# Optimization experiments

Measured on AMD Instinct MI355X. Metric: run time of the kernel, lower is better.

Reference implementation:

```python
import jax, jax.numpy as jnp
import numpy as np

N_NODES = 100000
N_EDGES = 1600000
H_FEATS = 128
OUT_CLASSES = 6


def setup_inputs() -> dict:
    key = jax.random.key(0)
    ks = jax.random.split(key, 9)
    h = jax.random.normal(ks[0], (N_NODES, H_FEATS), dtype=jnp.float32)
    src = jax.random.randint(ks[1], (N_EDGES,), 0, N_NODES)
    dst = jax.random.randint(ks[2], (N_EDGES,), 0, N_NODES)
    # torch nn.Linear convention: y = x @ W.T + b, W shape [out, in]
    W1 = jax.random.normal(ks[3], (64, 2 * H_FEATS), dtype=jnp.float32) * 0.05
    b1 = jax.random.normal(ks[4], (64,), dtype=jnp.float32) * 0.05
    W2 = jax.random.normal(ks[5], (32, 64), dtype=jnp.float32) * 0.05
    b2 = jax.random.normal(ks[6], (32,), dtype=jnp.float32) * 0.05
    W3 = jax.random.normal(ks[7], (OUT_CLASSES, 32), dtype=jnp.float32) * 0.05
    b3 = jax.random.normal(ks[8], (OUT_CLASSES,), dtype=jnp.float32) * 0.05
    return {"h": h, "src": src, "dst": dst, "W1": W1, "b1": b1,
            "W2": W2, "b2": b2, "W3": W3, "b3": b3}


def reference(h, src, dst, W1, b1, W2, b2, W3, b3):
    # Per-edge gather of src/dst node features, concat -> [E, 2*H]
    x = jnp.concatenate([h[src], h[dst]], axis=1)
    x = jax.nn.relu(x @ W1.T + b1)   # [E, 64]
    x = jax.nn.relu(x @ W2.T + b2)   # [E, 32]
    return x @ W3.T + b3             # [E, output_class]
```

## Files before the change

### kernel.cpp

```cpp
#include <hip/hip_runtime.h>
#include <hip/hip_bf16.h>
#include <stdint.h>


#define H 128

typedef short bf16x8 __attribute__((ext_vector_type(8)));
typedef float f32x4  __attribute__((ext_vector_type(4)));

__device__ __forceinline__ uint16_t f2bf(float f) {
    uint32_t u = __float_as_uint(f);
    return (uint16_t)((u + 0x7fffu + ((u >> 16) & 1u)) >> 16);
}
__device__ __forceinline__ float bf_lo(uint32_t u) { return __uint_as_float(u << 16); }
__device__ __forceinline__ float bf_hi(uint32_t u) { return __uint_as_float(u & 0xffff0000u); }
__device__ __forceinline__ uint32_t pk_bf16(float lo, float hi) {
    __hip_bfloat162 v = __float22bfloat162_rn(float2{lo, hi});
    return *reinterpret_cast<uint32_t*>(&v);
}

__global__ void prep_weights(const float* __restrict__ W1,
                             const float* __restrict__ W2,
                             const float* __restrict__ W3,
                             uint16_t* __restrict__ Bfrag,
                             uint16_t* __restrict__ EFrag)
{
    int t = blockIdx.x * blockDim.x + threadIdx.x;
    int stride = gridDim.x * blockDim.x;
    for (int i = t; i < 4 * 8 * 64 * 8; i += stride) {
        int j    = i & 7;
        int lane = (i >> 3) & 63;
        int nt   = (i >> 9) & 7;
        int kt   = (i >> 12);
        int k = kt * 32 + (lane >> 4) * 8 + j;
        int n = nt * 16 + (lane & 15);
        float v = (n < 64) ? W1[n * 256 + k] : W1[(n - 64) * 256 + 128 + k];
        Bfrag[i] = f2bf(v);
    }
    for (int i = t; i < 5 * 64 * 8; i += stride) {
        int j    = i & 7;
        int lane = (i >> 3) & 63;
        int f    = i >> 9;
        uint16_t v;
        if (f < 4) {
            int kt = f >> 1, nt = f & 1;
            int k = kt * 32 + (lane >> 4) * 8 + j;
            int n = nt * 16 + (lane & 15);
            v = f2bf(W2[n * 64 + k]);
        } else {
            int k = (lane >> 4) * 8 + j;
            int n = lane & 15;
            v = (n < 6) ? f2bf(W3[n * 32 + k]) : (uint16_t)0;
        }
        EFrag[i] = v;
    }
}

__global__ void __launch_bounds__(256) node_gemm(
    const float* __restrict__ h,
    const uint16_t* __restrict__ Bfrag,
    const float* __restrict__ b1,
    uint16_t* __restrict__ pre, int N)
{
    const int wave = threadIdx.x >> 6;
    const int lane = threadIdx.x & 63;
    const int n0 = (blockIdx.x * 4 + wave) * 16;
    if (n0 >= N) return;

    const int m    = lane & 15;
    const int quad = lane >> 4;

    int arow = n0 + m; if (arow >= N) arow = N - 1;
    const float* hrow = h + (size_t)arow * H + quad * 8;

    bf16x8 afr[4];
#pragma unroll
    for (int kt = 0; kt < 4; kt++) {
        float4 lo = *(const float4*)(hrow + kt * 32);
        float4 hi = *(const float4*)(hrow + kt * 32 + 4);
        bf16x8 a;
        a[0] = (short)f2bf(lo.x); a[1] = (short)f2bf(lo.y);
        a[2] = (short)f2bf(lo.z); a[3] = (short)f2bf(lo.w);
        a[4] = (short)f2bf(hi.x); a[5] = (short)f2bf(hi.y);
        a[6] = (short)f2bf(hi.z); a[7] = (short)f2bf(hi.w);
        afr[kt] = a;
    }

#pragma unroll
    for (int nt = 0; nt < 8; nt++) {
        f32x4 acc = {0.f, 0.f, 0.f, 0.f};
#pragma unroll
        for (int kt = 0; kt < 4; kt++) {
            bf16x8 bfr = *(const bf16x8*)(Bfrag + ((size_t)(kt * 8 + nt) * 64 + lane) * 8);
            acc = __builtin_amdgcn_mfma_f32_16x16x32_bf16(afr[kt], bfr, acc, 0, 0, 0);
        }
        const int ncol = nt * 16 + m;
        const float bv = (ncol < 64) ? b1[ncol] : 0.f;
#pragma unroll
        for (int r = 0; r < 4; r++) {
            const int node = n0 + quad * 4 + r;
            if (node < N)
                pre[(size_t)node * H + ncol] = f2bf(acc[r] + bv);
        }
    }
}

__global__ void __launch_bounds__(256, 2) edge_mlp(
    const uint16_t* __restrict__ pre,
    const int* __restrict__ src, const int* __restrict__ dst,
    const uint16_t* __restrict__ EFrag,
    const float* __restrict__ b2, const float* __restrict__ b3,
    float* __restrict__ out, long E)
{
    __shared__ uint16_t zbuf[4][64 * 40];

    const int wave = threadIdx.x >> 6;
    const int lane = threadIdx.x & 63;
    const int m15  = lane & 15;
    const int quad = lane >> 4;
    uint16_t* zw = &zbuf[wave][0];

    bf16x8 bL2[4], bL3;
#pragma unroll
    for (int f = 0; f < 4; f++) bL2[f] = *(const bf16x8*)(EFrag + (f * 64 + lane) * 8);
    bL3 = *(const bf16x8*)(EFrag + (4 * 64 + lane) * 8);
    const float vb2a = b2[m15];
    const float vb2b = b2[16 + m15];
    const float vb3  = (m15 < 6) ? b3[m15] : 0.f;

    const long e0 = (long)(blockIdx.x * 4 + wave) * 64;
    if (e0 >= E) return;

#pragma unroll
    for (int st = 0; st < 4; st++) {
        long e = e0 + st * 16 + m15;
        if (e >= E) e = E - 1;
        const int se = src[e], de = dst[e];
        const uint16_t* pa = pre + (size_t)se * H;
        const uint16_t* pb = pre + (size_t)de * H + 64;

        bf16x8 afr[2];
#pragma unroll
        for (int kt = 0; kt < 2; kt++) {
            uint4 ua = *(const uint4*)(pa + kt * 32 + quad * 8);
            uint4 ub = *(const uint4*)(pb + kt * 32 + quad * 8);
            float y0 = fmaxf(bf_lo(ua.x) + bf_lo(ub.x), 0.f);
            float y1 = fmaxf(bf_hi(ua.x) + bf_hi(ub.x), 0.f);
            float y2 = fmaxf(bf_lo(ua.y) + bf_lo(ub.y), 0.f);
            float y3 = fmaxf(bf_hi(ua.y) + bf_hi(ub.y), 0.f);
            float y4 = fmaxf(bf_lo(ua.z) + bf_lo(ub.z), 0.f);
            float y5 = fmaxf(bf_hi(ua.z) + bf_hi(ub.z), 0.f);
            float y6 = fmaxf(bf_lo(ua.w) + bf_lo(ub.w), 0.f);
            float y7 = fmaxf(bf_hi(ua.w) + bf_hi(ub.w), 0.f);
            union { bf16x8 v; uint32_t u[4]; } A;
            A.u[0] = pk_bf16(y0, y1);
            A.u[1] = pk_bf16(y2, y3);
            A.u[2] = pk_bf16(y4, y5);
            A.u[3] = pk_bf16(y6, y7);
            afr[kt] = A.v;
        }

#pragma unroll
        for (int nt = 0; nt < 2; nt++) {
            f32x4 acc = {0.f, 0.f, 0.f, 0.f};
            acc = __builtin_amdgcn_mfma_f32_16x16x32_bf16(afr[0], bL2[0 * 2 + nt], acc, 0, 0, 0);
            acc = __builtin_amdgcn_mfma_f32_16x16x32_bf16(afr[1], bL2[1 * 2 + nt], acc, 0, 0, 0);
            const float vb2 = nt ? vb2b : vb2a;
#pragma unroll
            for (int r = 0; r < 4; r++) {
                float z = fmaxf(acc[r] + vb2, 0.f);
                int el = st * 16 + quad * 4 + r;
                zw[el * 40 + nt * 16 + m15] = f2bf(z);
            }
        }
    }

#pragma unroll
    for (int st = 0; st < 4; st++) {
        bf16x8 a3 = *(const bf16x8*)(zw + (st * 16 + m15) * 40 + quad * 8);
        f32x4 o = {0.f, 0.f, 0.f, 0.f};
        o = __builtin_amdgcn_mfma_f32_16x16x32_bf16(a3, bL3, o, 0, 0, 0);
        if (m15 < 6) {
#pragma unroll
            for (int r = 0; r < 4; r++) {
                long e = e0 + st * 16 + quad * 4 + r;
                if (e < E) out[e * 6 + m15] = o[r] + vb3;
            }
        }
    }
}

extern "C" void kernel_launch(void* const* d_in, const int* in_sizes, int n_in,
                              void* d_out, int out_size, void* d_ws, size_t ws_size,
                              hipStream_t stream) {
    const float* h   = (const float*)d_in[0];
    const int*   src = (const int*)d_in[1];
    const int*   dst = (const int*)d_in[2];
    const float* W1  = (const float*)d_in[3];
    const float* b1  = (const float*)d_in[4];
    const float* W2  = (const float*)d_in[5];
    const float* b2  = (const float*)d_in[6];
    const float* W3  = (const float*)d_in[7];
    const float* b3  = (const float*)d_in[8];

    const int  N = in_sizes[0] / H;
    const long E = in_sizes[1];

    char* ws = (char*)d_ws;
    uint16_t* Bfrag = (uint16_t*)ws;
    uint16_t* EFrag = (uint16_t*)(ws + 64 * 1024);
    uint16_t* pre   = (uint16_t*)(ws + 128 * 1024);

    prep_weights<<<64, 256, 0, stream>>>(W1, W2, W3, Bfrag, EFrag);
    node_gemm<<<(N + 63) / 64, 256, 0, stream>>>(h, Bfrag, b1, pre, N);
    const int eblocks = (int)((E + 255) / 256);
    edge_mlp<<<eblocks, 256, 0, stream>>>(pre, src, dst, EFrag, b2, b3,
                                          (float*)d_out, E);
}
```

Before: 188.3 us.

## Drop weight-prep kernel and software-pipeline edge gathers over 128 edges per wave

Result: slower. 230.3 us (+22.3%).

```diff
diff --git a/kernel.cpp b/kernel.cpp
--- a/kernel.cpp
+++ b/kernel.cpp
@@ -18,47 +18,18 @@
     __hip_bfloat162 v = __float22bfloat162_rn(float2{lo, hi});
     return *reinterpret_cast<uint32_t*>(&v);
 }
-
-__global__ void prep_weights(const float* __restrict__ W1,
-                             const float* __restrict__ W2,
-                             const float* __restrict__ W3,
-                             uint16_t* __restrict__ Bfrag,
-                             uint16_t* __restrict__ EFrag)
-{
-    int t = blockIdx.x * blockDim.x + threadIdx.x;
-    int stride = gridDim.x * blockDim.x;
-    for (int i = t; i < 4 * 8 * 64 * 8; i += stride) {
-        int j    = i & 7;
-        int lane = (i >> 3) & 63;
-        int nt   = (i >> 9) & 7;
-        int kt   = (i >> 12);
-        int k = kt * 32 + (lane >> 4) * 8 + j;
-        int n = nt * 16 + (lane & 15);
-        float v = (n < 64) ? W1[n * 256 + k] : W1[(n - 64) * 256 + 128 + k];
-        Bfrag[i] = f2bf(v);
-    }
-    for (int i = t; i < 5 * 64 * 8; i += stride) {
-        int j    = i & 7;
-        int lane = (i >> 3) & 63;
-        int f    = i >> 9;
-        uint16_t v;
-        if (f < 4) {
-            int kt = f >> 1, nt = f & 1;
-            int k = kt * 32 + (lane >> 4) * 8 + j;
-            int n = nt * 16 + (lane & 15);
-            v = f2bf(W2[n * 64 + k]);
-        } else {
-            int k = (lane >> 4) * 8 + j;
-            int n = lane & 15;
-            v = (n < 6) ? f2bf(W3[n * 32 + k]) : (uint16_t)0;
-        }
-        EFrag[i] = v;
-    }
+__device__ __forceinline__ bf16x8 pack_frag(float4 lo, float4 hi) {
+    union { bf16x8 v; uint32_t u[4]; } A;
+    A.u[0] = pk_bf16(lo.x, lo.y);
+    A.u[1] = pk_bf16(lo.z, lo.w);
+    A.u[2] = pk_bf16(hi.x, hi.y);
+    A.u[3] = pk_bf16(hi.z, hi.w);
+    return A.v;
 }
 
 __global__ void __launch_bounds__(256) node_gemm(
     const float* __restrict__ h,
-    const uint16_t* __restrict__ Bfrag,
+    const float* __restrict__ W1,
     const float* __restrict__ b1,
     uint16_t* __restrict__ pre, int N)
 {
@@ -78,29 +49,33 @@
     for (int kt = 0; kt < 4; kt++) {
         float4 lo = *(const float4*)(hrow + kt * 32);
         float4 hi = *(const float4*)(hrow + kt * 32 + 4);
-        bf16x8 a;
-        a[0] = (short)f2bf(lo.x); a[1] = (short)f2bf(lo.y);
-        a[2] = (short)f2bf(lo.z); a[3] = (short)f2bf(lo.w);
-        a[4] = (short)f2bf(hi.x); a[5] = (short)f2bf(hi.y);
-        a[6] = (short)f2bf(hi.z); a[7] = (short)f2bf(hi.w);
-        afr[kt] = a;
-    }
+        afr[kt] = pack_frag(lo, hi);
+    }
+
+    float vb1[4];
+#pragma unroll
+    for (int nt = 0; nt < 4; nt++) vb1[nt] = b1[nt * 16 + m];
 
 #pragma unroll
     for (int nt = 0; nt < 8; nt++) {
+        const int n = nt * 16 + m;
+        const float* wrow = (n < 64) ? (W1 + (size_t)n * 256)
+                                     : (W1 + (size_t)(n - 64) * 256 + 128);
         f32x4 acc = {0.f, 0.f, 0.f, 0.f};
 #pragma unroll
         for (int kt = 0; kt < 4; kt++) {
-            bf16x8 bfr = *(const bf16x8*)(Bfrag + ((size_t)(kt * 8 + nt) * 64 + lane) * 8);
+            const float* wp = wrow + kt * 32 + quad * 8;
+            float4 lo = *(const float4*)wp;
+            float4 hi = *(const float4*)(wp + 4);
+            bf16x8 bfr = pack_frag(lo, hi);
             acc = __builtin_amdgcn_mfma_f32_16x16x32_bf16(afr[kt], bfr, acc, 0, 0, 0);
         }
-        const int ncol = nt * 16 + m;
-        const float bv = (ncol < 64) ? b1[ncol] : 0.f;
+        const float bv = (nt < 4) ? vb1[nt] : 0.f;
 #pragma unroll
         for (int r = 0; r < 4; r++) {
             const int node = n0 + quad * 4 + r;
             if (node < N)
-                pre[(size_t)node * H + ncol] = f2bf(acc[r] + bv);
+                pre[(size_t)node * H + n] = f2bf(acc[r] + bv);
         }
     }
 }
@@ -108,8 +83,8 @@
 __global__ void __launch_bounds__(256, 2) edge_mlp(
     const uint16_t* __restrict__ pre,
     const int* __restrict__ src, const int* __restrict__ dst,
-    const uint16_t* __restrict__ EFrag,
-    const float* __restrict__ b2, const float* __restrict__ b3,
+    const float* __restrict__ W2, const float* __restrict__ b2,
+    const float* __restrict__ W3, const float* __restrict__ b3,
     float* __restrict__ out, long E)
 {
     __shared__ uint16_t zbuf[4][64 * 40];
@@ -120,30 +95,67 @@
     const int quad = lane >> 4;
     uint16_t* zw = &zbuf[wave][0];
 
-    bf16x8 bL2[4], bL3;
-#pragma unroll
-    for (int f = 0; f < 4; f++) bL2[f] = *(const bf16x8*)(EFrag + (f * 64 + lane) * 8);
-    bL3 = *(const bf16x8*)(EFrag + (4 * 64 + lane) * 8);
+    bf16x8 bL2[4];
+#pragma unroll
+    for (int f = 0; f < 4; f++) {
+        const int kt = f >> 1, nt = f & 1;
+        const float* wp = W2 + (size_t)(nt * 16 + m15) * 64 + kt * 32 + quad * 8;
+        bL2[f] = pack_frag(*(const float4*)wp, *(const float4*)(wp + 4));
+    }
+    bf16x8 bL3;
+    {
+        const int n3 = (m15 < 6) ? m15 : 0;
+        const float* wp = W3 + (size_t)n3 * 32 + quad * 8;
+        union { bf16x8 v; uint32_t u[4]; } A;
+        float4 lo = *(const float4*)wp, hi = *(const float4*)(wp + 4);
+        A.u[0] = pk_bf16(lo.x, lo.y); A.u[1] = pk_bf16(lo.z, lo.w);
+        A.u[2] = pk_bf16(hi.x, hi.y); A.u[3] = pk_bf16(hi.z, hi.w);
+        if (m15 >= 6) { A.u[0] = A.u[1] = A.u[2] = A.u[3] = 0; }
+        bL3 = A.v;
+    }
     const float vb2a = b2[m15];
     const float vb2b = b2[16 + m15];
     const float vb3  = (m15 < 6) ? b3[m15] : 0.f;
 
-    const long e0 = (long)(blockIdx.x * 4 + wave) * 64;
-    if (e0 >= E) return;
-
-#pragma unroll
-    for (int st = 0; st < 4; st++) {
-        long e = e0 + st * 16 + m15;
+    const long base = (long)(blockIdx.x * 4 + wave) * 128;
+    if (base >= E) return;
+
+    int sidx[8], didx[8];
+#pragma unroll
+    for (int st = 0; st < 8; st++) {
+        long e = base + st * 16 + m15;
         if (e >= E) e = E - 1;
-        const int se = src[e], de = dst[e];
-        const uint16_t* pa = pre + (size_t)se * H;
-        const uint16_t* pb = pre + (size_t)de * H + 64;
+        sidx[st] = src[e]; didx[st] = dst[e];
+    }
+
+    uint4 ga[2][2], gb[2][2];
+    {
+        const uint16_t* pa = pre + (size_t)sidx[0] * H;
+        const uint16_t* pb = pre + (size_t)didx[0] * H + 64;
+        ga[0][0] = *(const uint4*)(pa + quad * 8);
+        ga[0][1] = *(const uint4*)(pa + 32 + quad * 8);
+        gb[0][0] = *(const uint4*)(pb + quad * 8);
+        gb[0][1] = *(const uint4*)(pb + 32 + quad * 8);
+    }
+
+#pragma unroll
+    for (int st = 0; st < 8; st++) {
+        const int cur = st & 1;
+        if (st < 7) {
+            const int nb = cur ^ 1;
+            const uint16_t* pa = pre + (size_t)sidx[st + 1] * H;
+            const uint16_t* pb = pre + (size_t)didx[st + 1] * H + 64;
+            ga[nb][0] = *(const uint4*)(pa + quad * 8);
+            ga[nb][1] = *(const uint4*)(pa + 32 + quad * 8);
+            gb[nb][0] = *(const uint4*)(pb + quad * 8);
+            gb[nb][1] = *(const uint4*)(pb + 32 + quad * 8);
+        }
 
         bf16x8 afr[2];
 #pragma unroll
         for (int kt = 0; kt < 2; kt++) {
-            uint4 ua = *(const uint4*)(pa + kt * 32 + quad * 8);
-            uint4 ub = *(const uint4*)(pb + kt * 32 + quad * 8);
+            uint4 ua = ga[cur][kt];
+            uint4 ub = gb[cur][kt];
             float y0 = fmaxf(bf_lo(ua.x) + bf_lo(ub.x), 0.f);
             float y1 = fmaxf(bf_hi(ua.x) + bf_hi(ub.x), 0.f);
             float y2 = fmaxf(bf_lo(ua.y) + bf_lo(ub.y), 0.f);
@@ -163,28 +175,31 @@
 #pragma unroll
         for (int nt = 0; nt < 2; nt++) {
             f32x4 acc = {0.f, 0.f, 0.f, 0.f};
-            acc = __builtin_amdgcn_mfma_f32_16x16x32_bf16(afr[0], bL2[0 * 2 + nt], acc, 0, 0, 0);
-            acc = __builtin_amdgcn_mfma_f32_16x16x32_bf16(afr[1], bL2[1 * 2 + nt], acc, 0, 0, 0);
+            acc = __builtin_amdgcn_mfma_f32_16x16x32_bf16(afr[0], bL2[nt],     acc, 0, 0, 0);
+            acc = __builtin_amdgcn_mfma_f32_16x16x32_bf16(afr[1], bL2[2 + nt], acc, 0, 0, 0);
             const float vb2 = nt ? vb2b : vb2a;
 #pragma unroll
             for (int r = 0; r < 4; r++) {
                 float z = fmaxf(acc[r] + vb2, 0.f);
-                int el = st * 16 + quad * 4 + r;
+                int el = (st & 3) * 16 + quad * 4 + r;
                 zw[el * 40 + nt * 16 + m15] = f2bf(z);
             }
         }
-    }
-
-#pragma unroll
-    for (int st = 0; st < 4; st++) {
-        bf16x8 a3 = *(const bf16x8*)(zw + (st * 16 + m15) * 40 + quad * 8);
-        f32x4 o = {0.f, 0.f, 0.f, 0.f};
-        o = __builtin_amdgcn_mfma_f32_16x16x32_bf16(a3, bL3, o, 0, 0, 0);
-        if (m15 < 6) {
-#pragma unroll
-            for (int r = 0; r < 4; r++) {
-                long e = e0 + st * 16 + quad * 4 + r;
-                if (e < E) out[e * 6 + m15] = o[r] + vb3;
+
+        if ((st & 3) == 3) {
+            const long gbase = base + (long)(st >> 2) * 64;
+#pragma unroll
+            for (int s2 = 0; s2 < 4; s2++) {
+                bf16x8 a3 = *(const bf16x8*)(zw + (s2 * 16 + m15) * 40 + quad * 8);
+                f32x4 o = {0.f, 0.f, 0.f, 0.f};
+                o = __builtin_amdgcn_mfma_f32_16x16x32_bf16(a3, bL3, o, 0, 0, 0);
+                if (m15 < 6) {
+#pragma unroll
+                    for (int r = 0; r < 4; r++) {
+                        long e = gbase + s2 * 16 + quad * 4 + r;
+                        if (e < E) out[e * 6 + m15] = o[r] + vb3;
+                    }
+                }
             }
         }
     }
@@ -206,14 +221,10 @@
     const int  N = in_sizes[0] / H;
     const long E = in_sizes[1];
 
-    char* ws = (char*)d_ws;
-    uint16_t* Bfrag = (uint16_t*)ws;
-    uint16_t* EFrag = (uint16_t*)(ws + 64 * 1024);
-    uint16_t* pre   = (uint16_t*)(ws + 128 * 1024);
-
-    prep_weights<<<64, 256, 0, stream>>>(W1, W2, W3, Bfrag, EFrag);
-    node_gemm<<<(N + 63) / 64, 256, 0, stream>>>(h, Bfrag, b1, pre, N);
-    const int eblocks = (int)((E + 255) / 256);
-    edge_mlp<<<eblocks, 256, 0, stream>>>(pre, src, dst, EFrag, b2, b3,
+    uint16_t* pre = (uint16_t*)d_ws;
+
+    node_gemm<<<(N + 63) / 64, 256, 0, stream>>>(h, W1, b1, pre, N);
+    const int eblocks = (int)((E + 511) / 512);
+    edge_mlp<<<eblocks, 256, 0, stream>>>(pre, src, dst, W2, b2, W3, b3,
                                           (float*)d_out, E);
 }
```

## Hoist all edge gathers up front, use packed bf16 add, double node rows per wave

Applied to the files above, without the earlier changes.

New measurement: 183.0 us. 2.8% less time.

```diff
diff --git a/kernel.cpp b/kernel.cpp
--- a/kernel.cpp
+++ b/kernel.cpp
@@ -12,11 +12,18 @@
     uint32_t u = __float_as_uint(f);
     return (uint16_t)((u + 0x7fffu + ((u >> 16) & 1u)) >> 16);
 }
-__device__ __forceinline__ float bf_lo(uint32_t u) { return __uint_as_float(u << 16); }
-__device__ __forceinline__ float bf_hi(uint32_t u) { return __uint_as_float(u & 0xffff0000u); }
 __device__ __forceinline__ uint32_t pk_bf16(float lo, float hi) {
     __hip_bfloat162 v = __float22bfloat162_rn(float2{lo, hi});
     return *reinterpret_cast<uint32_t*>(&v);
+}
+__device__ __forceinline__ uint32_t bfadd2_relu(uint32_t a, uint32_t b) {
+    __hip_bfloat162 x = *reinterpret_cast<__hip_bfloat162*>(&a);
+    __hip_bfloat162 y = *reinterpret_cast<__hip_bfloat162*>(&b);
+    __hip_bfloat162 s = __hadd2(x, y);
+    uint32_t zu = 0u;
+    __hip_bfloat162 zero = *reinterpret_cast<__hip_bfloat162*>(&zu);
+    __hip_bfloat162 r = __hmax2(s, zero);
+    return *reinterpret_cast<uint32_t*>(&r);
 }
 
 __global__ void prep_weights(const float* __restrict__ W1,
@@ -64,48 +71,51 @@
 {
     const int wave = threadIdx.x >> 6;
     const int lane = threadIdx.x & 63;
-    const int n0 = (blockIdx.x * 4 + wave) * 16;
+    const int n0 = (blockIdx.x * 4 + wave) * 32;
     if (n0 >= N) return;
 
     const int m    = lane & 15;
     const int quad = lane >> 4;
 
-    int arow = n0 + m; if (arow >= N) arow = N - 1;
-    const float* hrow = h + (size_t)arow * H + quad * 8;
-
-    bf16x8 afr[4];
-#pragma unroll
-    for (int kt = 0; kt < 4; kt++) {
-        float4 lo = *(const float4*)(hrow + kt * 32);
-        float4 hi = *(const float4*)(hrow + kt * 32 + 4);
-        bf16x8 a;
-        a[0] = (short)f2bf(lo.x); a[1] = (short)f2bf(lo.y);
-        a[2] = (short)f2bf(lo.z); a[3] = (short)f2bf(lo.w);
-        a[4] = (short)f2bf(hi.x); a[5] = (short)f2bf(hi.y);
-        a[6] = (short)f2bf(hi.z); a[7] = (short)f2bf(hi.w);
-        afr[kt] = a;
+    bf16x8 afr[2][4];
+#pragma unroll
+    for (int mt = 0; mt < 2; mt++) {
+        int arow = n0 + mt * 16 + m; if (arow >= N) arow = N - 1;
+        const float* hrow = h + (size_t)arow * H + quad * 8;
+#pragma unroll
+        for (int kt = 0; kt < 4; kt++) {
+            float4 lo = *(const float4*)(hrow + kt * 32);
+            float4 hi = *(const float4*)(hrow + kt * 32 + 4);
+            union { bf16x8 v; uint32_t u[4]; } A;
+            A.u[0] = pk_bf16(lo.x, lo.y); A.u[1] = pk_bf16(lo.z, lo.w);
+            A.u[2] = pk_bf16(hi.x, hi.y); A.u[3] = pk_bf16(hi.z, hi.w);
+            afr[mt][kt] = A.v;
+        }
     }
 
 #pragma unroll
     for (int nt = 0; nt < 8; nt++) {
-        f32x4 acc = {0.f, 0.f, 0.f, 0.f};
+        const int n = nt * 16 + m;
+        f32x4 acc0 = {0.f, 0.f, 0.f, 0.f};
+        f32x4 acc1 = {0.f, 0.f, 0.f, 0.f};
 #pragma unroll
         for (int kt = 0; kt < 4; kt++) {
             bf16x8 bfr = *(const bf16x8*)(Bfrag + ((size_t)(kt * 8 + nt) * 64 + lane) * 8);
-            acc = __builtin_amdgcn_mfma_f32_16x16x32_bf16(afr[kt], bfr, acc, 0, 0, 0);
-        }
-        const int ncol = nt * 16 + m;
-        const float bv = (ncol < 64) ? b1[ncol] : 0.f;
+            acc0 = __builtin_amdgcn_mfma_f32_16x16x32_bf16(afr[0][kt], bfr, acc0, 0, 0, 0);
+            acc1 = __builtin_amdgcn_mfma_f32_16x16x32_bf16(afr[1][kt], bfr, acc1, 0, 0, 0);
+        }
+        const float bv = (n < 64) ? b1[n] : 0.f;
 #pragma unroll
         for (int r = 0; r < 4; r++) {
-            const int node = n0 + quad * 4 + r;
-            if (node < N)
-                pre[(size_t)node * H + ncol] = f2bf(acc[r] + bv);
-        }
-    }
-}
-
-__global__ void __launch_bounds__(256, 2) edge_mlp(
+            const int node0 = n0 + quad * 4 + r;
+            if (node0 < N) pre[(size_t)node0 * H + n] = f2bf(acc0[r] + bv);
+            const int node1 = n0 + 16 + quad * 4 + r;
+            if (node1 < N) pre[(size_t)node1 * H + n] = f2bf(acc1[r] + bv);
+        }
+    }
+}
+
+__global__ void __launch_bounds__(256) edge_mlp(
     const uint16_t* __restrict__ pre,
     const int* __restrict__ src, const int* __restrict__ dst,
     const uint16_t* __restrict__ EFrag,
@@ -131,49 +141,70 @@
     const long e0 = (long)(blockIdx.x * 4 + wave) * 64;
     if (e0 >= E) return;
 
-#pragma unroll
-    for (int st = 0; st < 4; st++) {
-        long e = e0 + st * 16 + m15;
-        if (e >= E) e = E - 1;
-        const int se = src[e], de = dst[e];
-        const uint16_t* pa = pre + (size_t)se * H;
-        const uint16_t* pb = pre + (size_t)de * H + 64;
-
-        bf16x8 afr[2];
-#pragma unroll
-        for (int kt = 0; kt < 2; kt++) {
-            uint4 ua = *(const uint4*)(pa + kt * 32 + quad * 8);
-            uint4 ub = *(const uint4*)(pb + kt * 32 + quad * 8);
-            float y0 = fmaxf(bf_lo(ua.x) + bf_lo(ub.x), 0.f);
-            float y1 = fmaxf(bf_hi(ua.x) + bf_hi(ub.x), 0.f);
-            float y2 = fmaxf(bf_lo(ua.y) + bf_lo(ub.y), 0.f);
-            float y3 = fmaxf(bf_hi(ua.y) + bf_hi(ub.y), 0.f);
-            float y4 = fmaxf(bf_lo(ua.z) + bf_lo(ub.z), 0.f);
-            float y5 = fmaxf(bf_hi(ua.z) + bf_hi(ub.z), 0.f);
-            float y6 = fmaxf(bf_lo(ua.w) + bf_lo(ub.w), 0.f);
-            float y7 = fmaxf(bf_hi(ua.w) + bf_hi(ub.w), 0.f);
-            union { bf16x8 v; uint32_t u[4]; } A;
-            A.u[0] = pk_bf16(y0, y1);
-            A.u[1] = pk_bf16(y2, y3);
-            A.u[2] = pk_bf16(y4, y5);
-            A.u[3] = pk_bf16(y6, y7);
-            afr[kt] = A.v;
-        }
-
-#pragma unroll
-        for (int nt = 0; nt < 2; nt++) {
-            f32x4 acc = {0.f, 0.f, 0.f, 0.f};
-            acc = __builtin_amdgcn_mfma_f32_16x16x32_bf16(afr[0], bL2[0 * 2 + nt], acc, 0, 0, 0);
-            acc = __builtin_amdgcn_mfma_f32_16x16x32_bf16(afr[1], bL2[1 * 2 + nt], acc, 0, 0, 0);
-            const float vb2 = nt ? vb2b : vb2a;
-#pragma unroll
-            for (int r = 0; r < 4; r++) {
-                float z = fmaxf(acc[r] + vb2, 0.f);
-                int el = st * 16 + quad * 4 + r;
-                zw[el * 40 + nt * 16 + m15] = f2bf(z);
-            }
-        }
-    }
+    const char* preb = (const char*)pre;
+    uint32_t oa0, oa1, oa2, oa3, ob0, ob1, ob2, ob3;
+    {
+        long ea = e0 + m15;
+        long eb = (ea + 16 < E) ? ea + 16 : E - 1;
+        long ec = (ea + 32 < E) ? ea + 32 : E - 1;
+        long ed = (ea + 48 < E) ? ea + 48 : E - 1;
+        if (ea >= E) ea = E - 1;
+        oa0 = (uint32_t)src[ea] * 256u + (uint32_t)quad * 16u;
+        ob0 = (uint32_t)dst[ea] * 256u + 128u + (uint32_t)quad * 16u;
+        oa1 = (uint32_t)src[eb] * 256u + (uint32_t)quad * 16u;
+        ob1 = (uint32_t)dst[eb] * 256u + 128u + (uint32_t)quad * 16u;
+        oa2 = (uint32_t)src[ec] * 256u + (uint32_t)quad * 16u;
+        ob2 = (uint32_t)dst[ec] * 256u + 128u + (uint32_t)quad * 16u;
+        oa3 = (uint32_t)src[ed] * 256u + (uint32_t)quad * 16u;
+        ob3 = (uint32_t)dst[ed] * 256u + 128u + (uint32_t)quad * 16u;
+    }
+    uint4 a00 = *(const uint4*)(preb + oa0);
+    uint4 a01 = *(const uint4*)(preb + oa0 + 64);
+    uint4 b00 = *(const uint4*)(preb + ob0);
+    uint4 b01 = *(const uint4*)(preb + ob0 + 64);
+    uint4 a10 = *(const uint4*)(preb + oa1);
+    uint4 a11 = *(const uint4*)(preb + oa1 + 64);
+    uint4 b10 = *(const uint4*)(preb + ob1);
+    uint4 b11 = *(const uint4*)(preb + ob1 + 64);
+    uint4 a20 = *(const uint4*)(preb + oa2);
+    uint4 a21 = *(const uint4*)(preb + oa2 + 64);
+    uint4 b20 = *(const uint4*)(preb + ob2);
+    uint4 b21 = *(const uint4*)(preb + ob2 + 64);
+    uint4 a30 = *(const uint4*)(preb + oa3);
+    uint4 a31 = *(const uint4*)(preb + oa3 + 64);
+    uint4 b30 = *(const uint4*)(preb + ob3);
+    uint4 b31 = *(const uint4*)(preb + ob3 + 64);
+
+#define DO_SUBTILE(ST, UA0, UB0, UA1, UB1)                                        \
+    {                                                                             \
+        union { bf16x8 v; uint32_t u[4]; } A0, A1;                                \
+        A0.u[0] = bfadd2_relu(UA0.x, UB0.x);                                      \
+        A0.u[1] = bfadd2_relu(UA0.y, UB0.y);                                      \
+        A0.u[2] = bfadd2_relu(UA0.z, UB0.z);                                      \
+        A0.u[3] = bfadd2_relu(UA0.w, UB0.w);                                      \
+        A1.u[0] = bfadd2_relu(UA1.x, UB1.x);                                      \
+        A1.u[1] = bfadd2_relu(UA1.y, UB1.y);                                      \
+        A1.u[2] = bfadd2_relu(UA1.z, UB1.z);                                      \
+        A1.u[3] = bfadd2_relu(UA1.w, UB1.w);                                      \
+        _Pragma("unroll")                                                         \
+        for (int nt = 0; nt < 2; nt++) {                                          \
+            f32x4 acc = {0.f, 0.f, 0.f, 0.f};                                     \
+            acc = __builtin_amdgcn_mfma_f32_16x16x32_bf16(A0.v, bL2[nt], acc, 0, 0, 0); \
+            acc = __builtin_amdgcn_mfma_f32_16x16x32_bf16(A1.v, bL2[2 + nt], acc, 0, 0, 0); \
+            const float vb2 = nt ? vb2b : vb2a;                                   \
+            _Pragma("unroll")                                                     \
+            for (int r = 0; r < 4; r++) {                                         \
+                float z = fmaxf(acc[r] + vb2, 0.f);                               \
+                zw[((ST) * 16 + quad * 4 + r) * 40 + nt * 16 + m15] = f2bf(z);    \
+            }                                                                     \
+        }                                                                         \
+    }
+
+    DO_SUBTILE(0, a00, b00, a01, b01)
+    DO_SUBTILE(1, a10, b10, a11, b11)
+    DO_SUBTILE(2, a20, b20, a21, b21)
+    DO_SUBTILE(3, a30, b30, a31, b31)
+#undef DO_SUBTILE
 
 #pragma unroll
     for (int st = 0; st < 4; st++) {
@@ -212,7 +243,7 @@
     uint16_t* pre   = (uint16_t*)(ws + 128 * 1024);
 
     prep_weights<<<64, 256, 0, stream>>>(W1, W2, W3, Bfrag, EFrag);
-    node_gemm<<<(N + 63) / 64, 256, 0, stream>>>(h, Bfrag, b1, pre, N);
+    node_gemm<<<(N + 127) / 128, 256, 0, stream>>>(h, Bfrag, b1, pre, N);
     const int eblocks = (int)((E + 255) / 256);
     edge_mlp<<<eblocks, 256, 0, stream>>>(pre, src, dst, EFrag, b2, b3,
                                           (float*)d_out, E);
```
